# Kernel tuning notes

Hardware: AMD Instinct MI355X
Metric: run time of the kernel (lower is better)

## Reference

```python
import jax, jax.numpy as jnp
import numpy as np

B, N, C = 16, 2048, 3           # images, proposals/image, classes (incl. background)
K = 100                         # num_detections kept per class
SCORE_THRESH = 0.05
NMS_THRESH = 0.5
MIN_ANGLE = 10.0                # process_box min width (self.min_angle)
WX, WW = 1.0, 1.0               # box_coder reg_weights
NEG = jnp.float32(-1e9)


def setup_inputs() -> dict:
    key = jax.random.key(0)
    k1, k2, k3, k4 = jax.random.split(key, 4)
    class_logit = jax.random.normal(k1, (B, N, C), jnp.float32)
    box_regression = jax.random.normal(k2, (B, N, 2 * C), jnp.float32) * 0.1
    starts = jax.random.uniform(k3, (B, N), dtype=jnp.float32) * 300.0
    widths = jax.random.uniform(k4, (B, N), dtype=jnp.float32) * 50.0 + 12.0
    proposal = jnp.stack([starts, starts + widths], axis=-1)  # [B,N,2] 1-D intervals
    return {"class_logit": class_logit, "box_regression": box_regression,
            "proposal": proposal, "image_shape": 360}


def _decode(delta, prop):
    w = prop[:, 1] - prop[:, 0]
    ctr = prop[:, 0] + 0.5 * w
    dx = delta[:, 0] / WX
    dw = jnp.minimum(delta[:, 1] / WW, 4.0)  # clamp like torchvision
    pc = dx * w + ctr
    pw = jnp.exp(dw) * w
    return jnp.stack([pc - 0.5 * pw, pc + 0.5 * pw], axis=-1)  # [N,2]


def _iou_1d(a, b):
    inter = jnp.maximum(0.0, jnp.minimum(a[:, None, 1], b[None, :, 1])
                        - jnp.maximum(a[:, None, 0], b[None, :, 0]))
    union = (a[:, None, 1] - a[:, None, 0]) + (b[None, :, 1] - b[None, :, 0]) - inter
    return inter / jnp.maximum(union, 1e-8)  # [Na,Nb]


def _infer_one_class(score, delta, prop, image_shape):
    # score [N], delta [N,2], prop [N,2] -> [K,3] (start, end, score); invalid slots score=NEG
    box = _decode(delta, prop)
    lo = jnp.clip(box[:, 0], 0.0, image_shape)
    hi = jnp.clip(box[:, 1], 0.0, image_shape)
    box = jnp.stack([lo, hi], axis=-1)
    valid = ((hi - lo) >= MIN_ANGLE) & (score >= SCORE_THRESH)
    ms = jnp.where(valid, score, NEG)
    order = jnp.argsort(-ms)
    b = box[order]
    s = ms[order]
    sup = jax.lax.stop_gradient(_iou_1d(b, b)) > NMS_THRESH  # [N,N] bool
    idx = jnp.arange(N)

    def body(keep, i):  # greedy NMS in score order
        kill = sup[i] & keep[i] & (idx > i)
        return keep & ~kill, None

    keep0 = s > 0.5 * NEG
    keep, _ = jax.lax.scan(body, keep0, idx)
    ks = jnp.where(keep, s, NEG)
    top_s, top_i = jax.lax.top_k(ks, K)
    top_b = b[top_i]
    return jnp.concatenate([top_b, top_s[:, None]], axis=-1)  # [K,3]


def reference(class_logit, box_regression, proposal, image_shape):
    img = jnp.float32(image_shape)
    scores = jax.nn.softmax(class_logit, axis=-1)[..., 1:]        # [B,N,C-1] fg classes
    deltas = box_regression.reshape(B, N, C, 2)[:, :, 1:]         # [B,N,C-1,2]
    scores = jnp.moveaxis(scores, -1, 1)                          # [B,C-1,N]
    deltas = jnp.moveaxis(deltas, 2, 1)                           # [B,C-1,N,2]
    f = jax.vmap(jax.vmap(_infer_one_class, in_axes=(0, 0, None, None)),
                 in_axes=(0, 0, 0, None))
    return f(scores, deltas, proposal, img)  # [B, C-1, K, 3]
```

## Files before the change

### kernel.cpp

```cpp
#include <hip/hip_runtime.h>
#include <math.h>

#define B_IMG 16
#define N_PROP 2048
#define C_CLS 3
#define K_OUT 100
#define NTHREADS 1024
#define NWAVES (NTHREADS / 64)
#define NBLK64 (N_PROP / 64)
#define NUNITS (B_IMG * N_PROP)
#define NTHA 256
#define RUN 512

__device__ __forceinline__ unsigned long long shfl_xor_u64(unsigned long long v, int lx) {
    unsigned int lo = (unsigned int)__shfl_xor((int)(unsigned int)(v & 0xffffffffull), lx, 64);
    unsigned int hi = (unsigned int)__shfl_xor((int)(unsigned int)(v >> 32), lx, 64);
    return ((unsigned long long)hi << 32) | (unsigned long long)lo;
}
__device__ __forceinline__ float readlane_f(float v, int l) {
    return __int_as_float(__builtin_amdgcn_readlane(__float_as_int(v), l));
}
__device__ __forceinline__ unsigned long long readlane_u64(unsigned long long v, int l) {
    unsigned int lo = (unsigned int)__builtin_amdgcn_readlane((int)(unsigned int)(v & 0xffffffffull), l);
    unsigned int hi = (unsigned int)__builtin_amdgcn_readlane((int)(unsigned int)(v >> 32), l);
    return ((unsigned long long)hi << 32) | (unsigned long long)lo;
}
__device__ __forceinline__ bool iou_gt_half(float inter, float uni) {
    double b = (double)fmaxf(uni, 1e-8f);
    return (double)inter * 2.0 > b * 0x1.000001p0;
}
__device__ __forceinline__ float parse_imgf(int raw) {
    return (raw > 0 && raw < 1000000) ? (float)raw : __int_as_float(raw);
}

__global__ __launch_bounds__(NTHA)
void decode_sort_kernel(const float* __restrict__ class_logit,
                        const float* __restrict__ box_reg,
                        const float* __restrict__ proposal,
                        const int* __restrict__ image_shape_p,
                        unsigned long long* __restrict__ wskey,
                        float2* __restrict__ wbox)
{
#pragma clang fp contract(off)
    __shared__ unsigned long long skey[RUN];

    const int tid = threadIdx.x;
    const int lane = tid & 63;
    const int wid = tid >> 6;
    const int u = blockIdx.x >> 2;
    const int q = blockIdx.x & 3;
    const int img = u >> 1;
    const int cls = u & 1;
    const bool flip = (q & 1) != 0;
    const int off = q * RUN;
    const size_t base = (size_t)cls * NUNITS + (size_t)img * N_PROP;
    const float imgf = parse_imgf(image_shape_p[0]);

    for (int i = tid; i < RUN; i += NTHA) {
        const int n = off + i;
        const size_t g = (size_t)img * N_PROP + n;
        const float* lg = class_logit + g * C_CLS;
        float l0 = lg[0], l1 = lg[1], l2 = lg[2];
        float mx = fmaxf(l0, fmaxf(l1, l2));
        float e0 = (float)exp((double)(l0 - mx));
        float e1 = (float)exp((double)(l1 - mx));
        float e2 = (float)exp((double)(l2 - mx));
        float denom = (e0 + e1) + e2;
        float score = ((cls == 0) ? e1 : e2) / denom;

        const float* dr = box_reg + g * (2 * C_CLS) + 2 * (cls + 1);
        float dx = dr[0];
        float dw = fminf(dr[1], 4.0f);
        const float* pp = proposal + g * 2;
        float pA = pp[0], pB = pp[1];
        float w = pB - pA;
        float ctr = pA + 0.5f * w;
        float tt = dx * w;
        float pc = tt + ctr;
        float pw = (float)exp((double)dw) * w;
        float half = 0.5f * pw;
        float lo = pc - half;
        float hi = pc + half;
        lo = fminf(fmaxf(lo, 0.0f), imgf);
        hi = fminf(fmaxf(hi, 0.0f), imgf);
        bool valid = ((hi - lo) >= 10.0f) && (score >= 0.05f);
        float ms = valid ? score : -1e9f;
        wbox[base + n] = make_float2(lo, hi);
        unsigned int uu = __float_as_uint(ms);
        unsigned int e = (uu & 0x80000000u) ? ~uu : (uu | 0x80000000u);
        skey[i] = ((unsigned long long)e << 32) |
                  (unsigned long long)(0xFFFFFFFFu - (unsigned int)n);
    }
    __syncthreads();

    const int p0 = (wid << 7) | (lane << 1);
    const int p1 = p0 | 1;
    unsigned long long r0 = skey[p0], r1 = skey[p1];

    auto pass_inreg = [&](int k, int j) {
        bool desc = (((p0 & k) == 0) != flip);
        if (j == 1) {
            bool sw = desc ? (r0 < r1) : (r0 > r1);
            if (sw) { unsigned long long t = r0; r0 = r1; r1 = t; }
        } else {
            int lx = j >> 1;
            unsigned long long o0 = shfl_xor_u64(r0, lx);
            unsigned long long o1 = shfl_xor_u64(r1, lx);
            bool lower = ((p0 & j) == 0);
            bool takeMax = (lower == desc);
            r0 = takeMax ? (r0 > o0 ? r0 : o0) : (r0 < o0 ? r0 : o0);
            r1 = takeMax ? (r1 > o1 ? r1 : o1) : (r1 < o1 ? r1 : o1);
        }
    };

    for (int k = 2; k <= 128; k <<= 1)
        for (int j = k >> 1; j >= 1; j >>= 1)
            pass_inreg(k, j);

    for (int k = 256; k <= RUN; k <<= 1) {
        skey[p0] = r0; skey[p1] = r1;
        __syncthreads();
        for (int j = k >> 1; j >= 128; j >>= 1) {
            int i = ((tid & ~(j - 1)) << 1) | (tid & (j - 1));
            int part = i | j;
            unsigned long long a = skey[i], b = skey[part];
            bool desc_blk = (((i & k) == 0) != flip);
            bool sw = desc_blk ? (a < b) : (a > b);
            if (sw) { skey[i] = b; skey[part] = a; }
            __syncthreads();
        }
        r0 = skey[p0]; r1 = skey[p1];
        for (int j = 64; j >= 1; j >>= 1)
            pass_inreg(k, j);
    }
    wskey[base + off + p0] = r0;
    wskey[base + off + p1] = r1;
}

__global__ __launch_bounds__(NTHREADS)
void roiheads_kernel(const unsigned long long* __restrict__ wskey,
                     const float2* __restrict__ wbox,
                     float* __restrict__ out)
{
#pragma clang fp contract(off)
    __shared__ unsigned long long skey[N_PROP];
    __shared__ float slo[N_PROP], shi[N_PROP];
    __shared__ unsigned char keep[N_PROP];
    __shared__ unsigned short alv[2][N_PROP];
    __shared__ float clo[64], chi[64];
    __shared__ unsigned long long sup[64];
    __shared__ unsigned long long kmask[NBLK64];
    __shared__ int wsum[NWAVES];
    __shared__ int sh_nvalid;

    const int tid = threadIdx.x;
    const int lane = tid & 63;
    const int wid = tid >> 6;
    const int img = blockIdx.x >> 1;
    const int cls = blockIdx.x & 1;
    const size_t base = (size_t)cls * NUNITS + (size_t)img * N_PROP;

    if (tid == 0) sh_nvalid = 0;

    const int p0 = (wid << 7) | (lane << 1);
    const int p1 = p0 | 1;

    unsigned long long r0 = wskey[base + p0];
    unsigned long long r1 = wskey[base + p1];

    auto pass_inreg = [&](int k, int j) {
        if (j == 1) {
            bool desc = ((p0 & k) == 0);
            bool sw = desc ? (r0 < r1) : (r0 > r1);
            if (sw) { unsigned long long t = r0; r0 = r1; r1 = t; }
        } else {
            int lx = j >> 1;
            unsigned long long o0 = shfl_xor_u64(r0, lx);
            unsigned long long o1 = shfl_xor_u64(r1, lx);
            bool desc = ((p0 & k) == 0);
            bool lower = ((p0 & j) == 0);
            bool takeMax = (lower == desc);
            r0 = takeMax ? (r0 > o0 ? r0 : o0) : (r0 < o0 ? r0 : o0);
            r1 = takeMax ? (r1 > o1 ? r1 : o1) : (r1 < o1 ? r1 : o1);
        }
    };

    for (int k = 1024; k <= N_PROP; k <<= 1) {
        skey[p0] = r0; skey[p1] = r1;
        __syncthreads();
        for (int j = k >> 1; j >= 128; j >>= 1) {
            int i = ((tid & ~(j - 1)) << 1) | (tid & (j - 1));
            int part = i | j;
            unsigned long long a = skey[i], b = skey[part];
            bool desc_blk = ((i & k) == 0);
            bool sw = desc_blk ? (a < b) : (a > b);
            if (sw) { skey[i] = b; skey[part] = a; }
            __syncthreads();
        }
        r0 = skey[p0]; r1 = skey[p1];
        for (int j = 64; j >= 1; j >>= 1)
            pass_inreg(k, j);
    }
    skey[p0] = r0; skey[p1] = r1;
    __syncthreads();

    for (int i = tid; i < N_PROP; i += NTHREADS) {
        unsigned long long kk = skey[i];
        unsigned int e = (unsigned int)(kk >> 32);
        unsigned int sb = (e & 0x80000000u) ? (e & 0x7FFFFFFFu) : ~e;
        float s = __uint_as_float(sb);
        unsigned int n = 0xFFFFFFFFu - (unsigned int)(kk & 0xFFFFFFFFull);
        float2 bx = wbox[base + n];
        slo[i] = bx.x;
        shi[i] = bx.y;
        keep[i] = 0;
        bool v = (s > -5e8f);
        unsigned long long mb = __ballot(v);
        if (lane == 0) atomicAdd(&sh_nvalid, __popcll(mb));
        alv[0][i] = (unsigned short)i;
    }
    __syncthreads();

    int na = sh_nvalid;
    int cur = 0;
    int tk = 0;
    const unsigned long long below = (1ull << lane) - 1ull;

    while (na > 0) {
        const int m = (na < 64) ? na : 64;

        unsigned short cp = alv[cur][lane];
        bool cin = (lane < m);
        float qloc = cin ? slo[cp] : 0.0f;
        float qhic = cin ? shi[cp] : 0.0f;

#pragma unroll
        for (int rr4 = 0; rr4 < 4; ++rr4) {
            int rr = (wid << 2) | rr4;
            unsigned long long row = 0;
            if (rr < m) {
                unsigned short rp = alv[cur][rr];
                float rlo = slo[rp], rhi = shi[rp];
                float inter = fmaxf(fminf(rhi, qhic) - fmaxf(rlo, qloc), 0.0f);
                float uni = (rhi - rlo) + (qhic - qloc) - inter;
                bool kill = cin && (lane > rr) && iou_gt_half(inter, uni);
                row = __ballot(kill);
            }
            if (lane == 0) sup[rr] = row;
        }
        __syncthreads();

        unsigned long long rw = sup[lane];
        unsigned long long A = (m >= 64) ? ~0ull : ((1ull << m) - 1ull);
        unsigned long long kept = 0;
        while (A) {
            int c = __builtin_ctzll(A);
            kept |= (1ull << c);
            A &= ~(readlane_u64(rw, c) | (1ull << c));
        }
        const int cnt = __popcll(kept);

        if (wid == 0) {
            bool alive = cin && ((kept >> lane) & 1ull);
            if (alive) {
                keep[cp] = 1;
                int rank = __popcll(kept & below);
                clo[rank] = qloc; chi[rank] = qhic;
            }
        }
        __syncthreads();
        tk += cnt;
        if (tk >= K_OUT) break;

        float klo = 0.0f, khi = 0.0f;
        if (lane < cnt) { klo = clo[lane]; khi = chi[lane]; }
        int base2 = 0;
        for (int start = 64; start < na; start += NTHREADS) {
            int t2 = start + tid;
            unsigned short qq = 0;
            bool surv = false;
            if (t2 < na) {
                qq = alv[cur][t2];
                float qlo = slo[qq], qhi = shi[qq];
                float qw = qhi - qlo;
                bool dead = false;
                for (int r = 0; r < cnt; ++r) {
                    float cl = readlane_f(klo, r);
                    float ch = readlane_f(khi, r);
                    float inter = fmaxf(fminf(qhi, ch) - fmaxf(qlo, cl), 0.0f);
                    float uni = qw + (ch - cl) - inter;
                    dead |= iou_gt_half(inter, uni);
                }
                surv = !dead;
            }
            unsigned long long mb = __ballot(surv);
            if (lane == 0) wsum[wid] = __popcll(mb);
            __syncthreads();
            int off2 = base2, tot = base2;
            for (int w2 = 0; w2 < NWAVES; ++w2) {
                int c2 = wsum[w2];
                if (w2 < wid) off2 += c2;
                tot += c2;
            }
            if (surv) alv[cur ^ 1][off2 + __popcll(mb & below)] = qq;
            base2 = tot;
            __syncthreads();
        }
        na = base2;
        cur ^= 1;
    }

    for (int blk = wid; blk < NBLK64; blk += NWAVES) {
        bool kk = keep[blk * 64 + lane] != 0;
        unsigned long long mb = __ballot(kk);
        if (lane == 0) kmask[blk] = mb;
    }
    __syncthreads();
    {
        float* outp = out + (((size_t)img * 2 + cls) * K_OUT) * 3;
        for (int blk = wid; blk < NBLK64; blk += NWAVES) {
            int kc = 0, nc = 0, nk = 0;
            for (int b = 0; b < NBLK64; ++b) {
                int pc = __popcll(kmask[b]);
                nk += pc;
                if (b < blk) { kc += pc; nc += 64 - pc; }
            }
            if (kc >= K_OUT && nk + nc >= K_OUT && nc >= K_OUT) continue;
            int p = blk * 64 + lane;
            unsigned long long mb = kmask[blk];
            bool k = (mb >> lane) & 1ull;
            int rk = kc + __popcll(mb & below);
            int rn = nc + __popcll((~mb) & below);
            if (k) {
                if (rk < K_OUT) {
                    unsigned long long kk2 = skey[p];
                    unsigned int e = (unsigned int)(kk2 >> 32);
                    unsigned int sb = (e & 0x80000000u) ? (e & 0x7FFFFFFFu) : ~e;
                    outp[rk * 3 + 0] = slo[p];
                    outp[rk * 3 + 1] = shi[p];
                    outp[rk * 3 + 2] = __uint_as_float(sb);
                }
            } else {
                int oi = nk + rn;
                if (oi < K_OUT) {
                    outp[oi * 3 + 0] = slo[p];
                    outp[oi * 3 + 1] = shi[p];
                    outp[oi * 3 + 2] = -1e9f;
                }
            }
        }
    }
}

extern "C" void kernel_launch(void* const* d_in, const int* in_sizes, int n_in,
                              void* d_out, int out_size, void* d_ws, size_t ws_size,
                              hipStream_t stream) {
    const float* class_logit = (const float*)d_in[0];
    const float* box_reg     = (const float*)d_in[1];
    const float* prop        = (const float*)d_in[2];
    const int*   image_shape = (const int*)d_in[3];
    float* out = (float*)d_out;

    unsigned long long* wskey = (unsigned long long*)d_ws;
    float2* wbox = (float2*)((char*)d_ws + 2 * NUNITS * sizeof(unsigned long long));

    decode_sort_kernel<<<dim3(B_IMG * 2 * 4), dim3(NTHA), 0, stream>>>(
        class_logit, box_reg, prop, image_shape, wskey, wbox);
    roiheads_kernel<<<dim3(B_IMG * 2), dim3(NTHREADS), 0, stream>>>(
        wskey, wbox, out);
}
```

Baseline: 95.12 us.

## Widen NMS candidate window to 128 and sort 1024-element runs in stage one

The first kernel now sorts runs of 1024 keys with 512 threads, so the second kernel needs only the final bitonic merge stage. The greedy NMS loop now takes 128 candidates per iteration as two 64-lane halves, with a two-part suppression matrix and a two-phase resolve. The aim is fewer outer NMS iterations and barriers, and fewer sort passes in the single-block kernel. In exchange, each iteration builds a larger suppression matrix and runs a longer serial resolve, and the first kernel launches fewer, larger blocks.

```diff
diff --git a/kernel.cpp b/kernel.cpp
--- a/kernel.cpp
+++ b/kernel.cpp
@@ -9,8 +9,8 @@
 #define NWAVES (NTHREADS / 64)
 #define NBLK64 (N_PROP / 64)
 #define NUNITS (B_IMG * N_PROP)
-#define NTHA 256
-#define RUN 512
+#define NTHA 512
+#define RUN 1024
 
 __device__ __forceinline__ unsigned long long shfl_xor_u64(unsigned long long v, int lx) {
     unsigned int lo = (unsigned int)__shfl_xor((int)(unsigned int)(v & 0xffffffffull), lx, 64);
@@ -47,8 +47,8 @@
     const int tid = threadIdx.x;
     const int lane = tid & 63;
     const int wid = tid >> 6;
-    const int u = blockIdx.x >> 2;
-    const int q = blockIdx.x & 3;
+    const int u = blockIdx.x >> 1;
+    const int q = blockIdx.x & 1;
     const int img = u >> 1;
     const int cls = u & 1;
     const bool flip = (q & 1) != 0;
@@ -147,8 +147,8 @@
     __shared__ float slo[N_PROP], shi[N_PROP];
     __shared__ unsigned char keep[N_PROP];
     __shared__ unsigned short alv[2][N_PROP];
-    __shared__ float clo[64], chi[64];
-    __shared__ unsigned long long sup[64];
+    __shared__ float clo[128], chi[128];
+    __shared__ unsigned long long sup0[128], sup1[128];
     __shared__ unsigned long long kmask[NBLK64];
     __shared__ int wsum[NWAVES];
     __shared__ int sh_nvalid;
@@ -185,7 +185,8 @@
         }
     };
 
-    for (int k = 1024; k <= N_PROP; k <<= 1) {
+    {
+        const int k = N_PROP;
         skey[p0] = r0; skey[p1] = r1;
         __syncthreads();
         for (int j = k >> 1; j >= 128; j >>= 1) {
@@ -227,55 +228,79 @@
     const unsigned long long below = (1ull << lane) - 1ull;
 
     while (na > 0) {
-        const int m = (na < 64) ? na : 64;
-
-        unsigned short cp = alv[cur][lane];
-        bool cin = (lane < m);
-        float qloc = cin ? slo[cp] : 0.0f;
-        float qhic = cin ? shi[cp] : 0.0f;
+        const int m = (na < 128) ? na : 128;
+
+        unsigned short cp0 = alv[cur][lane];
+        unsigned short cp1 = alv[cur][64 + lane];
+        bool in0 = (lane < m), in1 = (64 + lane < m);
+        float q0l = in0 ? slo[cp0] : 0.0f, q0h = in0 ? shi[cp0] : 0.0f;
+        float q1l = in1 ? slo[cp1] : 0.0f, q1h = in1 ? shi[cp1] : 0.0f;
 
 #pragma unroll
-        for (int rr4 = 0; rr4 < 4; ++rr4) {
-            int rr = (wid << 2) | rr4;
+        for (int i = 0; i < 16; ++i) {
+            int u = (wid << 4) | i;
+            int r = u >> 1, h = u & 1;
             unsigned long long row = 0;
-            if (rr < m) {
-                unsigned short rp = alv[cur][rr];
-                float rlo = slo[rp], rhi = shi[rp];
-                float inter = fmaxf(fminf(rhi, qhic) - fmaxf(rlo, qloc), 0.0f);
-                float uni = (rhi - rlo) + (qhic - qloc) - inter;
-                bool kill = cin && (lane > rr) && iou_gt_half(inter, uni);
+            if (r < m && (((h << 6) | 63) > r)) {
+                float rl = readlane_f((r < 64) ? q0l : q1l, r & 63);
+                float rh = readlane_f((r < 64) ? q0h : q1h, r & 63);
+                float ql = h ? q1l : q0l, qh = h ? q1h : q0h;
+                bool inq = h ? in1 : in0;
+                float inter = fmaxf(fminf(rh, qh) - fmaxf(rl, ql), 0.0f);
+                float uni = (rh - rl) + (qh - ql) - inter;
+                int col = (h << 6) | lane;
+                bool kill = inq && (col > r) && iou_gt_half(inter, uni);
                 row = __ballot(kill);
             }
-            if (lane == 0) sup[rr] = row;
+            if (lane == 0) { if (h) sup1[r] = row; else sup0[r] = row; }
         }
         __syncthreads();
 
-        unsigned long long rw = sup[lane];
-        unsigned long long A = (m >= 64) ? ~0ull : ((1ull << m) - 1ull);
-        unsigned long long kept = 0;
-        while (A) {
-            int c = __builtin_ctzll(A);
-            kept |= (1ull << c);
-            A &= ~(readlane_u64(rw, c) | (1ull << c));
-        }
-        const int cnt = __popcll(kept);
+        unsigned long long rw00 = sup0[lane];
+        unsigned long long rw01 = sup1[lane];
+        unsigned long long rw11 = sup1[64 + lane];
+        unsigned long long A0 = (m >= 64) ? ~0ull : ((1ull << m) - 1ull);
+        unsigned long long A1 = (m > 64) ? ((m >= 128) ? ~0ull : ((1ull << (m - 64)) - 1ull)) : 0ull;
+        unsigned long long k0 = 0, k1 = 0;
+        while (A0) {
+            int c = __builtin_ctzll(A0);
+            k0 |= (1ull << c);
+            A0 &= ~(readlane_u64(rw00, c) | (1ull << c));
+            A1 &= ~readlane_u64(rw01, c);
+        }
+        while (A1) {
+            int c = __builtin_ctzll(A1);
+            k1 |= (1ull << c);
+            A1 &= ~(readlane_u64(rw11, c) | (1ull << c));
+        }
+        const int cnt0 = __popcll(k0);
+        const int cnt = cnt0 + __popcll(k1);
 
         if (wid == 0) {
-            bool alive = cin && ((kept >> lane) & 1ull);
+            bool alive = in0 && ((k0 >> lane) & 1ull);
             if (alive) {
-                keep[cp] = 1;
-                int rank = __popcll(kept & below);
-                clo[rank] = qloc; chi[rank] = qhic;
+                keep[cp0] = 1;
+                int rank = __popcll(k0 & below);
+                clo[rank] = q0l; chi[rank] = q0h;
+            }
+        } else if (wid == 1) {
+            bool alive = in1 && ((k1 >> lane) & 1ull);
+            if (alive) {
+                keep[cp1] = 1;
+                int rank = cnt0 + __popcll(k1 & below);
+                clo[rank] = q1l; chi[rank] = q1h;
             }
         }
         __syncthreads();
         tk += cnt;
         if (tk >= K_OUT) break;
 
-        float klo = 0.0f, khi = 0.0f;
-        if (lane < cnt) { klo = clo[lane]; khi = chi[lane]; }
+        float kl0 = 0.0f, kh0 = 0.0f, kl1 = 0.0f, kh1 = 0.0f;
+        if (lane < cnt) { kl0 = clo[lane]; kh0 = chi[lane]; }
+        if (64 + lane < cnt) { kl1 = clo[64 + lane]; kh1 = chi[64 + lane]; }
+        const int c1 = (cnt < 64) ? cnt : 64;
         int base2 = 0;
-        for (int start = 64; start < na; start += NTHREADS) {
+        for (int start = m; start < na; start += NTHREADS) {
             int t2 = start + tid;
             unsigned short qq = 0;
             bool surv = false;
@@ -284,9 +309,16 @@
                 float qlo = slo[qq], qhi = shi[qq];
                 float qw = qhi - qlo;
                 bool dead = false;
-                for (int r = 0; r < cnt; ++r) {
-                    float cl = readlane_f(klo, r);
-                    float ch = readlane_f(khi, r);
+                for (int r = 0; r < c1; ++r) {
+                    float cl = readlane_f(kl0, r);
+                    float ch = readlane_f(kh0, r);
+                    float inter = fmaxf(fminf(qhi, ch) - fmaxf(qlo, cl), 0.0f);
+                    float uni = qw + (ch - cl) - inter;
+                    dead |= iou_gt_half(inter, uni);
+                }
+                for (int r = 64; r < cnt; ++r) {
+                    float cl = readlane_f(kl1, r - 64);
+                    float ch = readlane_f(kh1, r - 64);
                     float inter = fmaxf(fminf(qhi, ch) - fmaxf(qlo, cl), 0.0f);
                     float uni = qw + (ch - cl) - inter;
                     dead |= iou_gt_half(inter, uni);
@@ -364,7 +396,7 @@
     unsigned long long* wskey = (unsigned long long*)d_ws;
     float2* wbox = (float2*)((char*)d_ws + 2 * NUNITS * sizeof(unsigned long long));
 
-    decode_sort_kernel<<<dim3(B_IMG * 2 * 4), dim3(NTHA), 0, stream>>>(
+    decode_sort_kernel<<<dim3(B_IMG * 2 * 2), dim3(NTHA), 0, stream>>>(
         class_logit, box_reg, prop, image_shape, wskey, wbox);
     roiheads_kernel<<<dim3(B_IMG * 2), dim3(NTHREADS), 0, stream>>>(
         wskey, wbox, out);
```

Measured after the change: 103.5 us. 8.8% more time.
